# Kernel optimization log

Hardware: AMD Instinct MI355X
Metric: run time of the kernel (lower is better)

Reference implementation:

```python
import jax, jax.numpy as jnp
import numpy as np

B, ENC_LEN, DEC_LEN = 4, 1024, 256
ENC_H, DEC_H, ATTN = 1024, 1024, 256


def setup_inputs() -> dict:
    key = jax.random.key(0)
    k1, k2, k3, k4, k5, k6 = jax.random.split(key, 6)
    scale = 0.02
    return {
        "encoded_seq": jax.random.normal(k1, (B, ENC_LEN, ENC_H), jnp.float32),
        "decoder_state": jax.random.normal(k2, (B, DEC_LEN, DEC_H), jnp.float32),
        "input_pad_mask": jnp.ones((B, ENC_LEN), jnp.float32),
        "Wh": jax.random.normal(k3, (ENC_H, ATTN), jnp.float32) * scale,
        "Ws": jax.random.normal(k4, (DEC_H, ATTN), jnp.float32) * scale,
        "bs": jax.random.normal(k5, (ATTN,), jnp.float32) * scale,
        "v": jax.random.normal(k6, (ATTN,), jnp.float32) * scale,
    }


def reference(encoded_seq, decoder_state, input_pad_mask, Wh, Ws, bs, v):
    # projections: [B, dec, A] and [B, enc, A]
    proj_dec = jnp.einsum('bdh,ha->bda', decoder_state, Ws) + bs
    proj_enc = jnp.einsum('beh,ha->bea', encoded_seq, Wh)
    # additive score: tanh(broadcast add) then dot with selector vector v
    added = jnp.tanh(proj_dec[:, :, None, :] + proj_enc[:, None, :, :])  # [B,dec,enc,A]
    attn_logits = jnp.einsum('bdea,a->bde', added, v)                    # [B,dec,enc]
    attn_weights = jax.nn.softmax(attn_logits, axis=-1)
    attn_weights2 = attn_weights * input_pad_mask[:, None, :]
    attn_renorm = attn_weights2 / jnp.sum(attn_weights2, axis=-1, keepdims=True)
    context = jnp.einsum('bde,beh->bdh', attn_renorm, encoded_seq)       # [B,dec,enc_h]
    return context, attn_renorm
```

## Files before the change

kernel.cpp:

```cpp
#include <hip/hip_runtime.h>
#include <hip/hip_bf16.h>

#define BB 4
#define ENC_LEN 1024
#define DEC_LEN 256
#define ENC_H 1024
#define ATTN_A 256

#define C2F 2.8853900817779268f

typedef short bf16x8 __attribute__((ext_vector_type(8)));
typedef float f32x4 __attribute__((ext_vector_type(4)));
typedef unsigned int u32x2 __attribute__((ext_vector_type(2)));

union F4U {
  float4 v;
  float f[4];
};
union Q2D {
  uint4 q;
  u32x2 d[2];
};
union BF8 {
  u32x2 d[2];
  bf16x8 v;
};

static __device__ __forceinline__ unsigned short f2bf(float x) {
  union {
    float f;
    unsigned int u;
  } c;
  c.f = x;
  unsigned int r = c.u + 0x7FFFu + ((c.u >> 16) & 1u);
  return (unsigned short)(r >> 16);
}

__global__ __launch_bounds__(256) void prep_k(const float* __restrict__ Wh,
                                              const float* __restrict__ Ws,
                                              const float* __restrict__ enc,
                                              unsigned short* __restrict__ WhT,
                                              unsigned short* __restrict__ WsT,
                                              unsigned short* __restrict__ encT) {
  __shared__ unsigned short T[64][68];
  const int wb = blockIdx.x;
  const float* in;
  unsigned short* out;
  int R, C, bx, by;
  if (wb < 128) {
    in = (wb < 64) ? Wh : Ws;
    out = (wb < 64) ? WhT : WsT;
    const int t = wb & 63;
    R = ENC_H;
    C = ATTN_A;
    bx = t & 3;
    by = t >> 2;
  } else {
    const int t = wb - 128;
    const int b = t >> 8;
    const int tt = t & 255;
    in = enc + (long)b * ENC_LEN * ENC_H;
    out = encT + (long)b * ENC_H * ENC_LEN;
    R = ENC_LEN;
    C = ENC_H;
    bx = tt & 15;
    by = tt >> 4;
  }
  const int r0 = by * 64;
  const int c0 = bx * 64;
  const int t = threadIdx.x;
  const int lr = t >> 4;
  const int lc4 = (t & 15) * 4;

#pragma unroll
  for (int p = 0; p < 4; ++p) {
    const int r = lr + p * 16;
    const float4 v = *(const float4*)&in[(long)(r0 + r) * C + c0 + lc4];
    ushort4 o;
    o.x = f2bf(v.x);
    o.y = f2bf(v.y);
    o.z = f2bf(v.z);
    o.w = f2bf(v.w);
    *(ushort4*)&T[r][lc4] = o;
  }
  __syncthreads();
#pragma unroll
  for (int p = 0; p < 4; ++p) {
    const int c = lr + p * 16;
    ushort4 o;
    o.x = T[lc4 + 0][c];
    o.y = T[lc4 + 1][c];
    o.z = T[lc4 + 2][c];
    o.w = T[lc4 + 3][c];
    *(ushort4*)&out[(long)(c0 + c) * R + r0 + lc4] = o;
  }
}

__global__ __launch_bounds__(256) void pgemm(const float* __restrict__ dec,
                                             const float* __restrict__ enc,
                                             const unsigned short* __restrict__ WsT,
                                             const unsigned short* __restrict__ WhT,
                                             float* __restrict__ pdP,
                                             float* __restrict__ peP) {
  __shared__ unsigned short As[64][36];
  __shared__ unsigned short Bs[64][36];
  __shared__ float Cs[64][68];

  const int s = blockIdx.z;
  const bool isPD = blockIdx.y < 16;
  const float* A = isPD ? dec : enc;
  const unsigned short* BT = isPD ? WsT : WhT;
  const int m0 = (isPD ? blockIdx.y : (blockIdx.y - 16)) * 64;
  const int n0 = blockIdx.x * 64;
  const int kb = s * 512;

  const int tid = threadIdx.x;
  const int lane = tid & 63;
  const int wave = tid >> 6;
  const int quad = lane >> 4;
  const int l16 = lane & 15;
  const int wm = (wave >> 1) * 32;
  const int wn = (wave & 1) * 32;
  const int sr = tid >> 2;
  const int sk = (tid & 3) * 8;

  f32x4 acc[2][2] = {{{0.f, 0.f, 0.f, 0.f}, {0.f, 0.f, 0.f, 0.f}},
                     {{0.f, 0.f, 0.f, 0.f}, {0.f, 0.f, 0.f, 0.f}}};

  const float* Ap = A + (long)(m0 + sr) * ENC_H + kb + sk;
  const unsigned short* Bp = BT + (long)(n0 + sr) * ENC_H + kb + sk;

  F4U a0, a1;
  Q2D bv;
  a0.v = *(const float4*)(Ap);
  a1.v = *(const float4*)(Ap + 4);
  bv.q = *(const uint4*)(Bp);

  for (int k0 = 0; k0 < 512; k0 += 32) {
    __syncthreads();
    Q2D av;
    av.q.x = (unsigned int)f2bf(a0.f[0]) | ((unsigned int)f2bf(a0.f[1]) << 16);
    av.q.y = (unsigned int)f2bf(a0.f[2]) | ((unsigned int)f2bf(a0.f[3]) << 16);
    av.q.z = (unsigned int)f2bf(a1.f[0]) | ((unsigned int)f2bf(a1.f[1]) << 16);
    av.q.w = (unsigned int)f2bf(a1.f[2]) | ((unsigned int)f2bf(a1.f[3]) << 16);
    *(u32x2*)&As[sr][sk] = av.d[0];
    *(u32x2*)&As[sr][sk + 4] = av.d[1];
    *(u32x2*)&Bs[sr][sk] = bv.d[0];
    *(u32x2*)&Bs[sr][sk + 4] = bv.d[1];
    const int kn = (k0 + 32 < 512) ? (k0 + 32) : 0;
    a0.v = *(const float4*)(Ap + kn);
    a1.v = *(const float4*)(Ap + kn + 4);
    bv.q = *(const uint4*)(Bp + kn);
    __syncthreads();

    bf16x8 af[2], bfr[2];
#pragma unroll
    for (int i = 0; i < 2; ++i) {
      BF8 t;
      t.d[0] = *(const u32x2*)&As[wm + i * 16 + l16][quad * 8];
      t.d[1] = *(const u32x2*)&As[wm + i * 16 + l16][quad * 8 + 4];
      af[i] = t.v;
    }
#pragma unroll
    for (int j = 0; j < 2; ++j) {
      BF8 t;
      t.d[0] = *(const u32x2*)&Bs[wn + j * 16 + l16][quad * 8];
      t.d[1] = *(const u32x2*)&Bs[wn + j * 16 + l16][quad * 8 + 4];
      bfr[j] = t.v;
    }
#pragma unroll
    for (int i = 0; i < 2; ++i)
#pragma unroll
      for (int j = 0; j < 2; ++j)
        acc[i][j] = __builtin_amdgcn_mfma_f32_16x16x32_bf16(af[i], bfr[j], acc[i][j],
                                                            0, 0, 0);
  }

  if (isPD) {
    float* out = pdP + (long)s * (1024 * ATTN_A);
#pragma unroll
    for (int j = 0; j < 2; ++j) {
      const int col = n0 + wn + j * 16 + l16;
#pragma unroll
      for (int i = 0; i < 2; ++i) {
        const int row = m0 + wm + i * 16 + quad * 4;
#pragma unroll
        for (int r = 0; r < 4; ++r)
          out[(long)(row + r) * ATTN_A + col] = C2F * acc[i][j][r];
      }
    }
  } else {
    __syncthreads();
#pragma unroll
    for (int i = 0; i < 2; ++i)
#pragma unroll
      for (int j = 0; j < 2; ++j)
#pragma unroll
        for (int r = 0; r < 4; ++r)
          Cs[wn + j * 16 + l16][wm + i * 16 + quad * 4 + r] = C2F * acc[i][j][r];
    __syncthreads();
    const int gb = m0 >> 10;
    const int e0 = m0 & 1023;
    float* out = peP + (long)s * (BB * ATTN_A * ENC_LEN);
#pragma unroll
    for (int p = 0; p < 4; ++p) {
      const int arow = (tid >> 4) + p * 16;
      const int e4 = (tid & 15) * 4;
      const float4 o = *(const float4*)&Cs[arow][e4];
      *(float4*)&out[(long)gb * (ATTN_A * ENC_LEN) + (long)(n0 + arow) * ENC_LEN +
                     e0 + e4] = o;
    }
  }
}

__global__ __launch_bounds__(256) void logits_k(const float* __restrict__ peP,
                                                const float* __restrict__ pdP,
                                                const float* __restrict__ v,
                                                const float* __restrict__ bs,
                                                float* __restrict__ p0,
                                                float* __restrict__ p1) {
  const int tid = threadIdx.x;
  const int e = blockIdx.x * 256 + tid;
  const int d0 = blockIdx.y * 8;
  const int b = blockIdx.z >> 1;
  const int a0 = (blockIdx.z & 1) * 128;

  __shared__ float Ed[128][8];
  __shared__ float vv[128];

  if (tid < 128) {
    const float cb = C2F * bs[a0 + tid];
#pragma unroll
    for (int dd = 0; dd < 8; ++dd) {
      const long idx = (long)(b * DEC_LEN + d0 + dd) * ATTN_A + a0 + tid;
      const float t = pdP[idx] + pdP[idx + 1024 * ATTN_A] + cb;
      Ed[tid][dd] = __builtin_amdgcn_exp2f(t);
    }
    vv[tid] = -2.0f * v[a0 + tid];
  }
  __syncthreads();

  float acc[8] = {0.f, 0.f, 0.f, 0.f, 0.f, 0.f, 0.f, 0.f};
  const float* pe0 = peP + (long)b * (ATTN_A * ENC_LEN) + (long)a0 * ENC_LEN + e;
  const float* pe1 = pe0 + (long)BB * ATTN_A * ENC_LEN;

  float pn0[4], pn1[4];
#pragma unroll
  for (int u = 0; u < 4; ++u) {
    pn0[u] = pe0[(long)u * ENC_LEN];
    pn1[u] = pe1[(long)u * ENC_LEN];
  }

  for (int a4 = 0; a4 < 128; a4 += 4) {
    float pes[4];
#pragma unroll
    for (int u = 0; u < 4; ++u) pes[u] = pn0[u] + pn1[u];
    const int an = (a4 + 4 < 128) ? (a4 + 4) : 0;
#pragma unroll
    for (int u = 0; u < 4; ++u) {
      pn0[u] = pe0[(long)(an + u) * ENC_LEN];
      pn1[u] = pe1[(long)(an + u) * ENC_LEN];
    }
#pragma unroll
    for (int u = 0; u < 4; ++u) {
      const float Ee = __builtin_amdgcn_exp2f(pes[u]);
      const float vu = vv[a4 + u];
      const float4 e0v = *(const float4*)&Ed[a4 + u][0];
      const float4 e1v = *(const float4*)&Ed[a4 + u][4];
      const float ed[8] = {e0v.x, e0v.y, e0v.z, e0v.w, e1v.x, e1v.y, e1v.z, e1v.w};
#pragma unroll
      for (int dd = 0; dd < 8; ++dd) {
        const float den = fmaf(ed[dd], Ee, 1.0f);
        const float r = __builtin_amdgcn_rcpf(den);
        acc[dd] = fmaf(vu, r, acc[dd]);
      }
    }
  }

  float* po = (blockIdx.z & 1) ? p1 : p0;
  const long base = ((long)(b * DEC_LEN + d0) * ENC_LEN) + e;
#pragma unroll
  for (int dd = 0; dd < 8; ++dd) po[base + (long)dd * ENC_LEN] = acc[dd];
}

__global__ __launch_bounds__(256) void softmax2_k(float* __restrict__ p0,
                                                  const float* __restrict__ p1,
                                                  const float* __restrict__ mask) {
  const int row = blockIdx.x;
  const int b = row >> 8;
  const int tid = threadIdx.x;
  float* rp = p0 + (long)row * ENC_LEN;
  const float* rq = p1 + (long)row * ENC_LEN;
  const float* mp = mask + b * ENC_LEN;

  float l[4], m[4];
#pragma unroll
  for (int j = 0; j < 4; ++j) {
    l[j] = rp[tid + 256 * j] + rq[tid + 256 * j];
    m[j] = mp[tid + 256 * j];
  }

  __shared__ float redmax[4];
  __shared__ float redsum[4];
  const int lane = tid & 63;
  const int wid = tid >> 6;

  float tm = fmaxf(fmaxf(l[0], l[1]), fmaxf(l[2], l[3]));
#pragma unroll
  for (int off = 1; off < 64; off <<= 1) tm = fmaxf(tm, __shfl_xor(tm, off, 64));
  if (lane == 0) redmax[wid] = tm;
  __syncthreads();
  const float rmax = fmaxf(fmaxf(redmax[0], redmax[1]), fmaxf(redmax[2], redmax[3]));

  const float LOG2E = 1.4426950408889634f;
  float p[4];
  float ts = 0.f;
#pragma unroll
  for (int j = 0; j < 4; ++j) {
    p[j] = __builtin_amdgcn_exp2f((l[j] - rmax) * LOG2E) * m[j];
    ts += p[j];
  }
#pragma unroll
  for (int off = 1; off < 64; off <<= 1) ts += __shfl_xor(ts, off, 64);
  if (lane == 0) redsum[wid] = ts;
  __syncthreads();
  const float rsum = redsum[0] + redsum[1] + redsum[2] + redsum[3];

  const float inv = 1.0f / rsum;
#pragma unroll
  for (int j = 0; j < 4; ++j) rp[tid + 256 * j] = p[j] * inv;
}

__global__ __launch_bounds__(256) void cgemm(const float* __restrict__ attn,
                                             const unsigned short* __restrict__ encT,
                                             float* __restrict__ cP) {
  __shared__ unsigned short As[64][36];
  __shared__ unsigned short Bs[64][36];

  const int b = blockIdx.z >> 1;
  const int s = blockIdx.z & 1;
  const int kb = s * 512;
  const float* A = attn + (long)b * DEC_LEN * ENC_LEN;
  const unsigned short* BT = encT + (long)b * ENC_H * ENC_LEN;
  float* C = cP + (long)s * (BB * DEC_LEN * ENC_H) + (long)b * DEC_LEN * ENC_H;

  const int tid = threadIdx.x;
  const int lane = tid & 63;
  const int wave = tid >> 6;
  const int quad = lane >> 4;
  const int l16 = lane & 15;
  const int wm = (wave >> 1) * 32;
  const int wn = (wave & 1) * 32;
  const int m0 = blockIdx.y * 64;
  const int n0 = blockIdx.x * 64;
  const int sr = tid >> 2;
  const int sk = (tid & 3) * 8;

  f32x4 acc[2][2] = {{{0.f, 0.f, 0.f, 0.f}, {0.f, 0.f, 0.f, 0.f}},
                     {{0.f, 0.f, 0.f, 0.f}, {0.f, 0.f, 0.f, 0.f}}};

  const float* Ap = A + (long)(m0 + sr) * ENC_LEN + kb + sk;
  const unsigned short* Bp = BT + (long)(n0 + sr) * ENC_LEN + kb + sk;

  F4U a0, a1;
  Q2D bv;
  a0.v = *(const float4*)(Ap);
  a1.v = *(const float4*)(Ap + 4);
  bv.q = *(const uint4*)(Bp);

  for (int k0 = 0; k0 < 512; k0 += 32) {
    __syncthreads();
    Q2D av;
    av.q.x = (unsigned int)f2bf(a0.f[0]) | ((unsigned int)f2bf(a0.f[1]) << 16);
    av.q.y = (unsigned int)f2bf(a0.f[2]) | ((unsigned int)f2bf(a0.f[3]) << 16);
    av.q.z = (unsigned int)f2bf(a1.f[0]) | ((unsigned int)f2bf(a1.f[1]) << 16);
    av.q.w = (unsigned int)f2bf(a1.f[2]) | ((unsigned int)f2bf(a1.f[3]) << 16);
    *(u32x2*)&As[sr][sk] = av.d[0];
    *(u32x2*)&As[sr][sk + 4] = av.d[1];
    *(u32x2*)&Bs[sr][sk] = bv.d[0];
    *(u32x2*)&Bs[sr][sk + 4] = bv.d[1];
    const int kn = (k0 + 32 < 512) ? (k0 + 32) : 0;
    a0.v = *(const float4*)(Ap + kn);
    a1.v = *(const float4*)(Ap + kn + 4);
    bv.q = *(const uint4*)(Bp + kn);
    __syncthreads();

    bf16x8 af[2], bfr[2];
#pragma unroll
    for (int i = 0; i < 2; ++i) {
      BF8 t;
      t.d[0] = *(const u32x2*)&As[wm + i * 16 + l16][quad * 8];
      t.d[1] = *(const u32x2*)&As[wm + i * 16 + l16][quad * 8 + 4];
      af[i] = t.v;
    }
#pragma unroll
    for (int j = 0; j < 2; ++j) {
      BF8 t;
      t.d[0] = *(const u32x2*)&Bs[wn + j * 16 + l16][quad * 8];
      t.d[1] = *(const u32x2*)&Bs[wn + j * 16 + l16][quad * 8 + 4];
      bfr[j] = t.v;
    }
#pragma unroll
    for (int i = 0; i < 2; ++i)
#pragma unroll
      for (int j = 0; j < 2; ++j)
        acc[i][j] = __builtin_amdgcn_mfma_f32_16x16x32_bf16(af[i], bfr[j], acc[i][j],
                                                            0, 0, 0);
  }

#pragma unroll
  for (int j = 0; j < 2; ++j) {
    const int col = n0 + wn + j * 16 + l16;
#pragma unroll
    for (int i = 0; i < 2; ++i) {
      const int row = m0 + wm + i * 16 + quad * 4;
#pragma unroll
      for (int r = 0; r < 4; ++r) C[(long)(row + r) * ENC_H + col] = acc[i][j][r];
    }
  }
}

__global__ __launch_bounds__(256) void creduce(const float* __restrict__ cP,
                                               float* __restrict__ ctx) {
  const long i = ((long)blockIdx.x * 256 + threadIdx.x) * 4;
  const float4 x = *(const float4*)&cP[i];
  const float4 y = *(const float4*)&cP[i + (long)BB * DEC_LEN * ENC_H];
  float4 o;
  o.x = x.x + y.x;
  o.y = x.y + y.y;
  o.z = x.z + y.z;
  o.w = x.w + y.w;
  *(float4*)&ctx[i] = o;
}

template <int OMODE, bool BIAS>
__global__ __launch_bounds__(256) void gemm64(const float* __restrict__ A,
                                              const float* __restrict__ B,
                                              const float* __restrict__ bias,
                                              float* __restrict__ C,
                                              int K, int lda, int ldb, int ldc,
                                              long sA, long sB, long sC) {
  const int bz = blockIdx.z;
  A += (long)bz * sA;
  B += (long)bz * sB;
  C += (long)bz * sC;

  const int tid = threadIdx.x;
  const int tx = tid & 15;
  const int ty = tid >> 4;

  __shared__ float As2[16][64];
  __shared__ float Bs2[16][64];

  float acc[4][4];
#pragma unroll
  for (int i = 0; i < 4; ++i)
#pragma unroll
    for (int j = 0; j < 4; ++j) acc[i][j] = 0.f;

  const int ar = tid >> 2;
  const int ak4 = (tid & 3) << 2;
  const int br = tid >> 4;
  const int bn4 = (tid & 15) << 2;

  const float* Aload = A + (long)(blockIdx.y * 64 + ar) * lda + ak4;
  const float* Bload = B + (long)br * ldb + blockIdx.x * 64 + bn4;

  for (int k0 = 0; k0 < K; k0 += 16) {
    const float4 av = *(const float4*)(Aload + k0);
    const float4 bv = *(const float4*)(Bload + (long)k0 * ldb);
    __syncthreads();
    As2[ak4 + 0][ar] = av.x;
    As2[ak4 + 1][ar] = av.y;
    As2[ak4 + 2][ar] = av.z;
    As2[ak4 + 3][ar] = av.w;
    *(float4*)&Bs2[br][bn4] = bv;
    __syncthreads();
#pragma unroll
    for (int kk = 0; kk < 16; ++kk) {
      const float4 a4 = *(const float4*)&As2[kk][ty << 2];
      const float4 b4 = *(const float4*)&Bs2[kk][tx << 2];
      const float am[4] = {a4.x, a4.y, a4.z, a4.w};
      const float bn[4] = {b4.x, b4.y, b4.z, b4.w};
#pragma unroll
      for (int i = 0; i < 4; ++i)
#pragma unroll
        for (int j = 0; j < 4; ++j) acc[i][j] = fmaf(am[i], bn[j], acc[i][j]);
    }
  }

  if (OMODE == 0) {
    const int row0 = blockIdx.y * 64 + (ty << 2);
    const int col0 = blockIdx.x * 64 + (tx << 2);
    float4 bb4 = make_float4(0.f, 0.f, 0.f, 0.f);
    if (BIAS) bb4 = *(const float4*)&bias[col0];
#pragma unroll
    for (int i = 0; i < 4; ++i) {
      float4 o;
      o.x = acc[i][0] + bb4.x;
      o.y = acc[i][1] + bb4.y;
      o.z = acc[i][2] + bb4.z;
      o.w = acc[i][3] + bb4.w;
      *(float4*)&C[(long)(row0 + i) * ldc + col0] = o;
    }
  } else {
#pragma unroll
    for (int i = 0; i < 4; ++i) {
      const int gr = blockIdx.y * 64 + (ty << 2) + i;
      const int b = gr >> 10;
      const int e = gr & 1023;
#pragma unroll
      for (int j = 0; j < 4; ++j) {
        const int col = blockIdx.x * 64 + (tx << 2) + j;
        C[(long)b * (ATTN_A * ENC_LEN) + (long)col * ENC_LEN + e] = acc[i][j];
      }
    }
  }
}

__global__ __launch_bounds__(256) void logits_fb(const float* __restrict__ peT,
                                                 const float* __restrict__ pd,
                                                 const float* __restrict__ v,
                                                 float* __restrict__ out) {
  const int tid = threadIdx.x;
  const int e = blockIdx.x * 256 + tid;
  const int d0 = blockIdx.y * 8;
  const int b = blockIdx.z;

  __shared__ float cpd[ATTN_A][8];
  __shared__ float vv[ATTN_A];

  {
    const int a = tid;
#pragma unroll
    for (int dd = 0; dd < 8; ++dd)
      cpd[a][dd] = C2F * pd[((b * DEC_LEN + d0 + dd) * ATTN_A) + a];
    vv[a] = -2.0f * v[a];
  }
  __syncthreads();

  float acc[8] = {0.f, 0.f, 0.f, 0.f, 0.f, 0.f, 0.f, 0.f};
  const float* pe = peT + (long)b * (ATTN_A * ENC_LEN) + e;

  for (int a = 0; a < ATTN_A; a += 4) {
    float pes[4];
#pragma unroll
    for (int u = 0; u < 4; ++u) pes[u] = pe[(long)(a + u) * ENC_LEN];
#pragma unroll
    for (int u = 0; u < 4; ++u) {
      const float cpe = C2F * pes[u];
      const float vu = vv[a + u];
      const float4 c0 = *(const float4*)&cpd[a + u][0];
      const float4 c1 = *(const float4*)&cpd[a + u][4];
      const float cd[8] = {c0.x, c0.y, c0.z, c0.w, c1.x, c1.y, c1.z, c1.w};
#pragma unroll
      for (int dd = 0; dd < 8; ++dd) {
        const float x = cd[dd] + cpe;
        const float ex = __builtin_amdgcn_exp2f(x);
        const float r = __builtin_amdgcn_rcpf(ex + 1.0f);
        acc[dd] = fmaf(vu, r, acc[dd]);
      }
    }
  }

  const long base = ((long)(b * DEC_LEN + d0) * ENC_LEN) + e;
#pragma unroll
  for (int dd = 0; dd < 8; ++dd) out[base + (long)dd * ENC_LEN] = acc[dd];
}

__global__ __launch_bounds__(256) void softmax_fb(float* __restrict__ attn,
                                                  const float* __restrict__ mask) {
  const int row = blockIdx.x;
  const int b = row >> 8;
  const int tid = threadIdx.x;
  float* rp = attn + (long)row * ENC_LEN;
  const float* mp = mask + b * ENC_LEN;

  float l[4], m[4];
#pragma unroll
  for (int j = 0; j < 4; ++j) {
    l[j] = rp[tid + 256 * j];
    m[j] = mp[tid + 256 * j];
  }

  __shared__ float redmax[4];
  __shared__ float redsum[4];
  const int lane = tid & 63;
  const int wid = tid >> 6;

  float tm = fmaxf(fmaxf(l[0], l[1]), fmaxf(l[2], l[3]));
#pragma unroll
  for (int off = 1; off < 64; off <<= 1) tm = fmaxf(tm, __shfl_xor(tm, off, 64));
  if (lane == 0) redmax[wid] = tm;
  __syncthreads();
  const float rmax = fmaxf(fmaxf(redmax[0], redmax[1]), fmaxf(redmax[2], redmax[3]));

  const float LOG2E = 1.4426950408889634f;
  float p[4];
  float ts = 0.f;
#pragma unroll
  for (int j = 0; j < 4; ++j) {
    p[j] = __builtin_amdgcn_exp2f((l[j] - rmax) * LOG2E) * m[j];
    ts += p[j];
  }
#pragma unroll
  for (int off = 1; off < 64; off <<= 1) ts += __shfl_xor(ts, off, 64);
  if (lane == 0) redsum[wid] = ts;
  __syncthreads();
  const float rsum = redsum[0] + redsum[1] + redsum[2] + redsum[3];

  const float inv = 1.0f / rsum;
#pragma unroll
  for (int j = 0; j < 4; ++j) rp[tid + 256 * j] = p[j] * inv;
}

extern "C" void kernel_launch(void* const* d_in, const int* in_sizes, int n_in,
                              void* d_out, int out_size, void* d_ws, size_t ws_size,
                              hipStream_t stream) {
  const float* enc = (const float*)d_in[0];
  const float* dec = (const float*)d_in[1];
  const float* mask = (const float*)d_in[2];
  const float* Wh = (const float*)d_in[3];
  const float* Ws = (const float*)d_in[4];
  const float* bs = (const float*)d_in[5];
  const float* v = (const float*)d_in[6];

  float* ctx = (float*)d_out;
  float* attn = ctx + (long)BB * DEC_LEN * ENC_H;

  const long N_PD = 2L * 1024 * ATTN_A;
  const long N_PE = 2L * BB * ATTN_A * ENC_LEN;
  const long N_P1 = (long)BB * DEC_LEN * ENC_LEN;
  const long N_CP = 2L * BB * DEC_LEN * ENC_H;
  const size_t FAST_WS = (N_PD + N_PE + N_P1 + N_CP) * 4 +
                         ((long)BB * ENC_H * ENC_LEN + 2L * ATTN_A * ENC_H) * 2;

  if (ws_size >= FAST_WS) {
    float* pdP = (float*)d_ws;
    float* peP = pdP + N_PD;
    float* p1 = peP + N_PE;
    float* cP = p1 + N_P1;
    unsigned short* encT = (unsigned short*)(cP + N_CP);
    unsigned short* WhT = encT + (long)BB * ENC_H * ENC_LEN;
    unsigned short* WsT = WhT + (long)ATTN_A * ENC_H;

    prep_k<<<dim3(1152, 1, 1), 256, 0, stream>>>(Wh, Ws, enc, WhT, WsT, encT);
    pgemm<<<dim3(4, 80, 2), 256, 0, stream>>>(dec, enc, WsT, WhT, pdP, peP);
    logits_k<<<dim3(4, 32, BB * 2), 256, 0, stream>>>(peP, pdP, v, bs, attn, p1);
    softmax2_k<<<dim3(BB * DEC_LEN, 1, 1), 256, 0, stream>>>(attn, p1, mask);
    cgemm<<<dim3(16, 4, BB * 2), 256, 0, stream>>>(attn, encT, cP);
    creduce<<<dim3(1024, 1, 1), 256, 0, stream>>>(cP, ctx);
  } else {
    float* pd = (float*)d_ws;
    float* peT = pd + (long)BB * DEC_LEN * ATTN_A;

    gemm64<0, true><<<dim3(ATTN_A / 64, (BB * DEC_LEN) / 64, 1), 256, 0, stream>>>(
        dec, Ws, bs, pd, ENC_H, ENC_H, ATTN_A, ATTN_A, 0, 0, 0);
    gemm64<1, false><<<dim3(ATTN_A / 64, (BB * ENC_LEN) / 64, 1), 256, 0, stream>>>(
        enc, Wh, nullptr, peT, ENC_H, ENC_H, ATTN_A, 0, 0, 0, 0);
    logits_fb<<<dim3(ENC_LEN / 256, DEC_LEN / 8, BB), 256, 0, stream>>>(peT, pd, v,
                                                                        attn);
    softmax_fb<<<dim3(BB * DEC_LEN, 1, 1), 256, 0, stream>>>(attn, mask);
    gemm64<0, false><<<dim3(ENC_H / 64, DEC_LEN / 64, BB), 256, 0, stream>>>(
        attn, enc, nullptr, ctx, ENC_LEN, ENC_LEN, ENC_H, ENC_H,
        (long)DEC_LEN * ENC_LEN, (long)ENC_LEN * ENC_H, (long)DEC_LEN * ENC_H);
  }
}
```

Baseline: 150.8 us.

## Pre-convert GEMM A-operands to bf16 and batch four rcp into one

The prep kernel now also writes bf16 copies of the encoder and decoder inputs, and softmax writes a bf16 copy of the attention weights. The projection and context GEMMs therefore load bf16 directly instead of loading fp32 and converting inside the main loop, which halves their A-operand traffic. The logits loop combines four reciprocal terms into a single fraction, so it needs one rcp per four attention columns instead of four. The costs are extra workspace, extra bf16 write traffic, and a possible risk of overflow or precision loss in the product of four denominators.

Result: faster. 143.3 us (-5.0%).

```diff
diff --git a/kernel.cpp b/kernel.cpp
--- a/kernel.cpp
+++ b/kernel.cpp
@@ -13,10 +13,6 @@
 typedef float f32x4 __attribute__((ext_vector_type(4)));
 typedef unsigned int u32x2 __attribute__((ext_vector_type(2)));
 
-union F4U {
-  float4 v;
-  float f[4];
-};
 union Q2D {
   uint4 q;
   u32x2 d[2];
@@ -36,31 +32,55 @@
   return (unsigned short)(r >> 16);
 }
 
-__global__ __launch_bounds__(256) void prep_k(const float* __restrict__ Wh,
-                                              const float* __restrict__ Ws,
-                                              const float* __restrict__ enc,
-                                              unsigned short* __restrict__ WhT,
-                                              unsigned short* __restrict__ WsT,
-                                              unsigned short* __restrict__ encT) {
+__global__ __launch_bounds__(256) void prep_k(
+    const float* __restrict__ Wh, const float* __restrict__ Ws,
+    const float* __restrict__ enc, const float* __restrict__ dec,
+    unsigned short* __restrict__ WhT, unsigned short* __restrict__ WsT,
+    unsigned short* __restrict__ encT, unsigned short* __restrict__ encB,
+    unsigned short* __restrict__ decB) {
   __shared__ unsigned short T[64][68];
   const int wb = blockIdx.x;
+  const int t = threadIdx.x;
+  const int lr = t >> 4;
+  const int lc4 = (t & 15) * 4;
+
+  if (wb >= 1152) {
+    const int q = wb - 1152;
+    const int r0 = (q >> 4) * 64;
+    const int c0 = (q & 15) * 64;
+#pragma unroll
+    for (int p = 0; p < 4; ++p) {
+      const int r = lr + p * 16;
+      const float4 v = *(const float4*)&dec[(long)(r0 + r) * ENC_H + c0 + lc4];
+      ushort4 o;
+      o.x = f2bf(v.x);
+      o.y = f2bf(v.y);
+      o.z = f2bf(v.z);
+      o.w = f2bf(v.w);
+      *(ushort4*)&decB[(long)(r0 + r) * ENC_H + c0 + lc4] = o;
+    }
+    return;
+  }
+
   const float* in;
   unsigned short* out;
+  unsigned short* out2 = nullptr;
   int R, C, bx, by;
   if (wb < 128) {
     in = (wb < 64) ? Wh : Ws;
     out = (wb < 64) ? WhT : WsT;
-    const int t = wb & 63;
+    const int tt = wb & 63;
     R = ENC_H;
     C = ATTN_A;
-    bx = t & 3;
-    by = t >> 2;
+    bx = tt & 3;
+    by = tt >> 2;
   } else {
-    const int t = wb - 128;
-    const int b = t >> 8;
-    const int tt = t & 255;
+    const int tt0 = wb - 128;
+    const int b = tt0 >> 8;
+    const int tt = tt0 & 255;
     in = enc + (long)b * ENC_LEN * ENC_H;
     out = encT + (long)b * ENC_H * ENC_LEN;
+    out2 = encB + (long)b * ENC_LEN * ENC_H;
     R = ENC_LEN;
     C = ENC_H;
     bx = tt & 15;
@@ -68,9 +88,6 @@
   }
   const int r0 = by * 64;
   const int c0 = bx * 64;
-  const int t = threadIdx.x;
-  const int lr = t >> 4;
-  const int lc4 = (t & 15) * 4;
 
 #pragma unroll
   for (int p = 0; p < 4; ++p) {
@@ -82,6 +99,7 @@
     o.z = f2bf(v.z);
     o.w = f2bf(v.w);
     *(ushort4*)&T[r][lc4] = o;
+    if (out2) *(ushort4*)&out2[(long)(r0 + r) * C + c0 + lc4] = o;
   }
   __syncthreads();
 #pragma unroll
@@ -96,8 +114,8 @@
   }
 }
 
-__global__ __launch_bounds__(256) void pgemm(const float* __restrict__ dec,
-                                             const float* __restrict__ enc,
+__global__ __launch_bounds__(256) void pgemm(const unsigned short* __restrict__ decB,
+                                             const unsigned short* __restrict__ encB,
                                              const unsigned short* __restrict__ WsT,
                                              const unsigned short* __restrict__ WhT,
                                              float* __restrict__ pdP,
@@ -108,7 +126,7 @@
 
   const int s = blockIdx.z;
   const bool isPD = blockIdx.y < 16;
-  const float* A = isPD ? dec : enc;
+  const unsigned short* A = isPD ? decB : encB;
   const unsigned short* BT = isPD ? WsT : WhT;
   const int m0 = (isPD ? blockIdx.y : (blockIdx.y - 16)) * 64;
   const int n0 = blockIdx.x * 64;
@@ -127,29 +145,21 @@
   f32x4 acc[2][2] = {{{0.f, 0.f, 0.f, 0.f}, {0.f, 0.f, 0.f, 0.f}},
                      {{0.f, 0.f, 0.f, 0.f}, {0.f, 0.f, 0.f, 0.f}}};
 
-  const float* Ap = A + (long)(m0 + sr) * ENC_H + kb + sk;
+  const unsigned short* Ap = A + (long)(m0 + sr) * ENC_H + kb + sk;
   const unsigned short* Bp = BT + (long)(n0 + sr) * ENC_H + kb + sk;
 
-  F4U a0, a1;
-  Q2D bv;
-  a0.v = *(const float4*)(Ap);
-  a1.v = *(const float4*)(Ap + 4);
+  Q2D av, bv;
+  av.q = *(const uint4*)(Ap);
   bv.q = *(const uint4*)(Bp);
 
   for (int k0 = 0; k0 < 512; k0 += 32) {
     __syncthreads();
-    Q2D av;
-    av.q.x = (unsigned int)f2bf(a0.f[0]) | ((unsigned int)f2bf(a0.f[1]) << 16);
-    av.q.y = (unsigned int)f2bf(a0.f[2]) | ((unsigned int)f2bf(a0.f[3]) << 16);
-    av.q.z = (unsigned int)f2bf(a1.f[0]) | ((unsigned int)f2bf(a1.f[1]) << 16);
-    av.q.w = (unsigned int)f2bf(a1.f[2]) | ((unsigned int)f2bf(a1.f[3]) << 16);
     *(u32x2*)&As[sr][sk] = av.d[0];
     *(u32x2*)&As[sr][sk + 4] = av.d[1];
     *(u32x2*)&Bs[sr][sk] = bv.d[0];
     *(u32x2*)&Bs[sr][sk + 4] = bv.d[1];
     const int kn = (k0 + 32 < 512) ? (k0 + 32) : 0;
-    a0.v = *(const float4*)(Ap + kn);
-    a1.v = *(const float4*)(Ap + kn + 4);
+    av.q = *(const uint4*)(Ap + kn);
     bv.q = *(const uint4*)(Bp + kn);
     __syncthreads();
 
@@ -252,28 +262,49 @@
   }
 
   for (int a4 = 0; a4 < 128; a4 += 4) {
-    float pes[4];
-#pragma unroll
-    for (int u = 0; u < 4; ++u) pes[u] = pn0[u] + pn1[u];
+    float Ee[4];
+#pragma unroll
+    for (int u = 0; u < 4; ++u) Ee[u] = __builtin_amdgcn_exp2f(pn0[u] + pn1[u]);
     const int an = (a4 + 4 < 128) ? (a4 + 4) : 0;
 #pragma unroll
     for (int u = 0; u < 4; ++u) {
       pn0[u] = pe0[(long)(an + u) * ENC_LEN];
       pn1[u] = pe1[(long)(an + u) * ENC_LEN];
     }
+    const float4 v4 = *(const float4*)&vv[a4];
+
+    float ed[4][8];
 #pragma unroll
     for (int u = 0; u < 4; ++u) {
-      const float Ee = __builtin_amdgcn_exp2f(pes[u]);
-      const float vu = vv[a4 + u];
       const float4 e0v = *(const float4*)&Ed[a4 + u][0];
       const float4 e1v = *(const float4*)&Ed[a4 + u][4];
-      const float ed[8] = {e0v.x, e0v.y, e0v.z, e0v.w, e1v.x, e1v.y, e1v.z, e1v.w};
-#pragma unroll
-      for (int dd = 0; dd < 8; ++dd) {
-        const float den = fmaf(ed[dd], Ee, 1.0f);
-        const float r = __builtin_amdgcn_rcpf(den);
-        acc[dd] = fmaf(vu, r, acc[dd]);
-      }
+      ed[u][0] = e0v.x;
+      ed[u][1] = e0v.y;
+      ed[u][2] = e0v.z;
+      ed[u][3] = e0v.w;
+      ed[u][4] = e1v.x;
+      ed[u][5] = e1v.y;
+      ed[u][6] = e1v.z;
+      ed[u][7] = e1v.w;
+    }
+
+#pragma unroll
+    for (int dd = 0; dd < 8; ++dd) {
+      const float dn0 = fmaf(ed[0][dd], Ee[0], 1.0f);
+      const float dn1 = fmaf(ed[1][dd], Ee[1], 1.0f);
+      const float dn2 = fmaf(ed[2][dd], Ee[2], 1.0f);
+      const float dn3 = fmaf(ed[3][dd], Ee[3], 1.0f);
+      const float x12 = dn0 * dn1;
+      const float x34 = dn2 * dn3;
+      float t1 = v4.x * dn1;
+      t1 = fmaf(v4.y, dn0, t1);
+      float t2 = v4.z * dn3;
+      t2 = fmaf(v4.w, dn2, t2);
+      float num = t1 * x34;
+      num = fmaf(t2, x12, num);
+      const float D = x12 * x34;
+      const float r = __builtin_amdgcn_rcpf(D);
+      acc[dd] = fmaf(num, r, acc[dd]);
     }
   }
 
@@ -285,13 +316,15 @@
 
 __global__ __launch_bounds__(256) void softmax2_k(float* __restrict__ p0,
                                                   const float* __restrict__ p1,
-                                                  const float* __restrict__ mask) {
+                                                  const float* __restrict__ mask,
+                                                  unsigned short* __restrict__ attnB) {
   const int row = blockIdx.x;
   const int b = row >> 8;
   const int tid = threadIdx.x;
   float* rp = p0 + (long)row * ENC_LEN;
   const float* rq = p1 + (long)row * ENC_LEN;
   const float* mp = mask + b * ENC_LEN;
+  unsigned short* rb = attnB + (long)row * ENC_LEN;
 
   float l[4], m[4];
 #pragma unroll
@@ -328,10 +361,14 @@
 
   const float inv = 1.0f / rsum;
 #pragma unroll
-  for (int j = 0; j < 4; ++j) rp[tid + 256 * j] = p[j] * inv;
-}
-
-__global__ __launch_bounds__(256) void cgemm(const float* __restrict__ attn,
+  for (int j = 0; j < 4; ++j) {
+    const float w = p[j] * inv;
+    rp[tid + 256 * j] = w;
+    rb[tid + 256 * j] = f2bf(w);
+  }
+}
+
+__global__ __launch_bounds__(256) void cgemm(const unsigned short* __restrict__ attnB,
                                              const unsigned short* __restrict__ encT,
                                              float* __restrict__ cP) {
   __shared__ unsigned short As[64][36];
@@ -340,7 +377,7 @@
   const int b = blockIdx.z >> 1;
   const int s = blockIdx.z & 1;
   const int kb = s * 512;
-  const float* A = attn + (long)b * DEC_LEN * ENC_LEN;
+  const unsigned short* A = attnB + (long)b * DEC_LEN * ENC_LEN;
   const unsigned short* BT = encT + (long)b * ENC_H * ENC_LEN;
   float* C = cP + (long)s * (BB * DEC_LEN * ENC_H) + (long)b * DEC_LEN * ENC_H;
 
@@ -359,29 +396,21 @@
   f32x4 acc[2][2] = {{{0.f, 0.f, 0.f, 0.f}, {0.f, 0.f, 0.f, 0.f}},
                      {{0.f, 0.f, 0.f, 0.f}, {0.f, 0.f, 0.f, 0.f}}};
 
-  const float* Ap = A + (long)(m0 + sr) * ENC_LEN + kb + sk;
+  const unsigned short* Ap = A + (long)(m0 + sr) * ENC_LEN + kb + sk;
   const unsigned short* Bp = BT + (long)(n0 + sr) * ENC_LEN + kb + sk;
 
-  F4U a0, a1;
-  Q2D bv;
-  a0.v = *(const float4*)(Ap);
-  a1.v = *(const float4*)(Ap + 4);
+  Q2D av, bv;
+  av.q = *(const uint4*)(Ap);
   bv.q = *(const uint4*)(Bp);
 
   for (int k0 = 0; k0 < 512; k0 += 32) {
     __syncthreads();
-    Q2D av;
-    av.q.x = (unsigned int)f2bf(a0.f[0]) | ((unsigned int)f2bf(a0.f[1]) << 16);
-    av.q.y = (unsigned int)f2bf(a0.f[2]) | ((unsigned int)f2bf(a0.f[3]) << 16);
-    av.q.z = (unsigned int)f2bf(a1.f[0]) | ((unsigned int)f2bf(a1.f[1]) << 16);
-    av.q.w = (unsigned int)f2bf(a1.f[2]) | ((unsigned int)f2bf(a1.f[3]) << 16);
     *(u32x2*)&As[sr][sk] = av.d[0];
     *(u32x2*)&As[sr][sk + 4] = av.d[1];
     *(u32x2*)&Bs[sr][sk] = bv.d[0];
     *(u32x2*)&Bs[sr][sk + 4] = bv.d[1];
     const int kn = (k0 + 32 < 512) ? (k0 + 32) : 0;
-    a0.v = *(const float4*)(Ap + kn);
-    a1.v = *(const float4*)(Ap + kn + 4);
+    av.q = *(const uint4*)(Ap + kn);
     bv.q = *(const uint4*)(Bp + kn);
     __syncthreads();
 
@@ -632,8 +661,12 @@
   const long N_PE = 2L * BB * ATTN_A * ENC_LEN;
   const long N_P1 = (long)BB * DEC_LEN * ENC_LEN;
   const long N_CP = 2L * BB * DEC_LEN * ENC_H;
+  const long N_ENC = (long)BB * ENC_H * ENC_LEN;
+  const long N_W = (long)ATTN_A * ENC_H;
+  const long N_DEC = 1024L * ENC_H;
+  const long N_ATT = (long)BB * DEC_LEN * ENC_LEN;
   const size_t FAST_WS = (N_PD + N_PE + N_P1 + N_CP) * 4 +
-                         ((long)BB * ENC_H * ENC_LEN + 2L * ATTN_A * ENC_H) * 2;
+                         (N_ENC + 2 * N_W + N_ENC + N_DEC + N_ATT) * 2;
 
   if (ws_size >= FAST_WS) {
     float* pdP = (float*)d_ws;
@@ -641,14 +674,18 @@
     float* p1 = peP + N_PE;
     float* cP = p1 + N_P1;
     unsigned short* encT = (unsigned short*)(cP + N_CP);
-    unsigned short* WhT = encT + (long)BB * ENC_H * ENC_LEN;
-    unsigned short* WsT = WhT + (long)ATTN_A * ENC_H;
-
-    prep_k<<<dim3(1152, 1, 1), 256, 0, stream>>>(Wh, Ws, enc, WhT, WsT, encT);
-    pgemm<<<dim3(4, 80, 2), 256, 0, stream>>>(dec, enc, WsT, WhT, pdP, peP);
+    unsigned short* WhT = encT + N_ENC;
+    unsigned short* WsT = WhT + N_W;
+    unsigned short* encB = WsT + N_W;
+    unsigned short* decB = encB + N_ENC;
+    unsigned short* attnB = decB + N_DEC;
+
+    prep_k<<<dim3(1408, 1, 1), 256, 0, stream>>>(Wh, Ws, enc, dec, WhT, WsT, encT,
+                                                 encB, decB);
+    pgemm<<<dim3(4, 80, 2), 256, 0, stream>>>(decB, encB, WsT, WhT, pdP, peP);
     logits_k<<<dim3(4, 32, BB * 2), 256, 0, stream>>>(peP, pdP, v, bs, attn, p1);
-    softmax2_k<<<dim3(BB * DEC_LEN, 1, 1), 256, 0, stream>>>(attn, p1, mask);
-    cgemm<<<dim3(16, 4, BB * 2), 256, 0, stream>>>(attn, encT, cP);
+    softmax2_k<<<dim3(BB * DEC_LEN, 1, 1), 256, 0, stream>>>(attn, p1, mask, attnB);
+    cgemm<<<dim3(16, 4, BB * 2), 256, 0, stream>>>(attnB, encT, cP);
     creduce<<<dim3(1024, 1, 1), 256, 0, stream>>>(cP, ctx);
   } else {
     float* pd = (float*)d_ws;
```
